# Kernel optimization log

Measured on AMD Instinct MI355X. Metric: run time of the kernel, lower is better.

## Reference

```python
import jax, jax.numpy as jnp
import numpy as np
import math

N = 512            # batch
D = 512            # in_features (embedding dim)
C = 50000          # out_features (num classes)
S = 30.0           # scale
M = 0.5            # margin
COS_M = math.cos(M)
SIN_M = math.sin(M)
TH = math.cos(math.pi - M)
MM = math.sin(math.pi - M) * M


def _l2norm(x, eps=1e-12):
    # torch F.normalize: x / max(||x||_2, eps) along dim=1
    n = jnp.sqrt(jnp.sum(x * x, axis=1, keepdims=True))
    return x / jnp.maximum(n, eps)


def setup_inputs() -> dict:
    key = jax.random.key(0)
    k1, k2, k3 = jax.random.split(key, 3)
    logits = jax.random.normal(k1, (N, D), dtype=jnp.float32)
    labels = jax.random.randint(k2, (N,), 0, C, dtype=jnp.int64)
    # xavier_uniform over (C, D): bound = sqrt(6/(C+D))
    bound = math.sqrt(6.0 / (C + D))
    weight = jax.random.uniform(k3, (C, D), dtype=jnp.float32, minval=-bound, maxval=bound)
    return {"logits": logits, "labels": labels, "weight": weight}


def reference(logits, labels, weight):
    x = _l2norm(logits)                      # [N, D]
    w = _l2norm(weight)                      # [C, D]
    cosine = jnp.einsum('nd,cd->nc', x, w)   # [N, C]
    sine = jnp.sqrt(jnp.clip(1.0 + 1e-7 - cosine * cosine, 0.0, 1.0))
    phi = cosine * COS_M - sine * SIN_M
    # easy_margin=False branch
    phi = jnp.where(cosine > TH, phi, cosine - MM)
    onehot = jax.nn.one_hot(labels, C, dtype=cosine.dtype)  # [N, C]
    output = (onehot * phi + (1.0 - onehot) * cosine) * S
    # CrossEntropyLoss(reduction='none') then .mean()
    logp = jax.nn.log_softmax(output, axis=1)
    loss_per = -jnp.take_along_axis(logp, labels[:, None], axis=1)[:, 0]
    loss = jnp.mean(loss_per)
    return output, loss
```

## Files before the change

### kernel.cpp

```cpp
#include <hip/hip_runtime.h>
#include <stdint.h>

#define N_B   512
#define D_K   512
#define C_N   50000
#define C_PAD 50048
#define BM    256
#define BN    128
#define BK    32
#define NCB   391
#define NWG   (NCB * 2)
#define NT    16

#define S_SCALE 30.0f
#define COS_Mc  0.87758256189037276f
#define SIN_Mc  0.47942553860420301f
#define TH_Cc  (-0.87758256189037276f)
#define MM_Cc   0.23971276930210156f
#define NEG_BIG (-3.0e38f)

typedef __attribute__((ext_vector_type(8))) __bf16 bf16x8;
typedef __attribute__((ext_vector_type(4))) float  f32x4;

__device__ __forceinline__ unsigned short f2bf(float f) {
    union { float f; unsigned u; } v; v.f = f;
    unsigned r = v.u + 0x7FFFu + ((v.u >> 16) & 1u);
    return (unsigned short)(r >> 16);
}

__device__ __forceinline__ void gl2lds16(const void* g, void* l) {
    __builtin_amdgcn_global_load_lds(
        (__attribute__((address_space(1))) unsigned int*)(g),
        (__attribute__((address_space(3))) unsigned int*)(l),
        16, 0, 0);
}

__global__ __launch_bounds__(256) void prep_all_kernel(
        const float* __restrict__ x, unsigned short* __restrict__ xb,
        float* __restrict__ invx,
        const float* __restrict__ w, unsigned short* __restrict__ wb,
        float* __restrict__ invw)
{
    const int wave = threadIdx.x >> 6, lane = threadIdx.x & 63;
    const int l15 = lane & 15, sub = lane >> 4;
    const float* src; unsigned short* dstb; float* inv; int row, nvalid;
    if (blockIdx.x < 32) {
        src = x; dstb = xb; inv = invx; nvalid = N_B;
        row = blockIdx.x * 16 + wave * 4 + sub;
    } else {
        src = w; dstb = wb; inv = invw; nvalid = C_N;
        row = (blockIdx.x - 32) * 16 + wave * 4 + sub;
    }
    unsigned short* drow = dstb + (size_t)row * D_K;
    if (row < nvalid) {
        const float4* s4 = (const float4*)(src + (size_t)row * D_K);
        float4 v[8];
        #pragma unroll
        for (int k = 0; k < 8; k++) v[k] = s4[l15 + 16 * k];
        float ss = 0.f;
        #pragma unroll
        for (int k = 0; k < 8; k++)
            ss += v[k].x * v[k].x + v[k].y * v[k].y
                + v[k].z * v[k].z + v[k].w * v[k].w;
        #pragma unroll
        for (int off = 1; off < 16; off <<= 1) ss += __shfl_xor(ss, off, 64);
        if (l15 == 0) inv[row] = 1.0f / fmaxf(sqrtf(ss), 1e-12f);
        #pragma unroll
        for (int k = 0; k < 8; k++) {
            uint2 o;
            o.x = (unsigned)f2bf(v[k].x) | ((unsigned)f2bf(v[k].y) << 16);
            o.y = (unsigned)f2bf(v[k].z) | ((unsigned)f2bf(v[k].w) << 16);
            *(uint2*)(drow + (l15 + 16 * k) * 4) = o;
        }
    } else {
        uint2 z = make_uint2(0u, 0u);
        #pragma unroll
        for (int k = 0; k < 8; k++) *(uint2*)(drow + (l15 + 16 * k) * 4) = z;
        if (l15 == 0) inv[row] = 0.0f;
    }
}

__global__ __launch_bounds__(512, 4) void gemm_margin_kernel(
        const unsigned short* __restrict__ xb, const unsigned short* __restrict__ wb,
        const float* __restrict__ invx, const float* __restrict__ invw,
        const int* __restrict__ labels, float* __restrict__ out,
        float* __restrict__ m_part, float* __restrict__ s_part)
{
    const int orig = blockIdx.x;
    const int qch = NWG >> 3, rch = NWG & 7;
    const int xcd = orig & 7, idx = orig >> 3;
    const int wg = (xcd < rch ? xcd * (qch + 1)
                              : rch * (qch + 1) + (xcd - rch) * qch) + idx;
    const int cb = wg >> 1, rb = wg & 1;
    const int m0 = rb * BM, c0 = cb * BN;
    const int tid = threadIdx.x;
    const int lane = tid & 63, wave = tid >> 6;
    const int wm = wave >> 1, wn = wave & 1;
    const int l15 = lane & 15, q = lane >> 4;

    __shared__ __align__(16) unsigned short As[2][BM * BK];
    __shared__ __align__(16) unsigned short Bs[2][BN * BK];
    __shared__ float s_invx[BM];
    __shared__ float s_invw[BN];
    __shared__ int   s_lab[BM];
    float* sm  = (float*)&As[0][0];
    float* ssm = sm + 2 * BM;

    f32x4 zero4 = {0.f, 0.f, 0.f, 0.f};
    f32x4 acc[4][4];
    #pragma unroll
    for (int i = 0; i < 4; i++)
        #pragma unroll
        for (int j = 0; j < 4; j++) acc[i][j] = zero4;

    const int srow   = tid >> 2;
    const int pchunk = tid & 3;
    const int lch0 = pchunk ^ ((srow >> 1) & 3);
    const int lch1 = pchunk ^ (((srow + 128) >> 1) & 3);

    const unsigned short* gA0 = xb + (size_t)(m0 + srow)       * D_K + lch0 * 8;
    const unsigned short* gA1 = xb + (size_t)(m0 + srow + 128) * D_K + lch1 * 8;
    const unsigned short* gB0 = wb + (size_t)(c0 + srow)       * D_K + lch0 * 8;

    const int offA0 = srow * BK + pchunk * 8;
    const int offA1 = (srow + 128) * BK + pchunk * 8;
    const int offB0 = srow * BK + pchunk * 8;

    int aoff[4], boff[4];
    #pragma unroll
    for (int i = 0; i < 4; i++) {
        int Ra = wm * 64 + i * 16 + l15;
        aoff[i] = Ra * BK + (q ^ ((Ra >> 1) & 3)) * 8;
        int Rb = wn * 64 + i * 16 + l15;
        boff[i] = Rb * BK + (q ^ ((Rb >> 1) & 3)) * 8;
    }

#define STAGE(b, k0) do {                       \
        gl2lds16(gA0 + (k0), &As[b][offA0]);    \
        gl2lds16(gA1 + (k0), &As[b][offA1]);    \
        gl2lds16(gB0 + (k0), &Bs[b][offB0]);    \
    } while (0)

#define COMPUTE(b) do {                                                       \
        bf16x8 af_[4], bf_[4];                                                \
        _Pragma("unroll")                                                     \
        for (int i = 0; i < 4; i++) af_[i] = *(const bf16x8*)(&As[b][aoff[i]]); \
        _Pragma("unroll")                                                     \
        for (int i = 0; i < 4; i++) bf_[i] = *(const bf16x8*)(&Bs[b][boff[i]]); \
        _Pragma("unroll")                                                     \
        for (int mi = 0; mi < 4; mi++)                                        \
            _Pragma("unroll")                                                 \
            for (int ni = 0; ni < 4; ni++)                                    \
                acc[mi][ni] = __builtin_amdgcn_mfma_f32_16x16x32_bf16(        \
                                  af_[mi], bf_[ni], acc[mi][ni], 0, 0, 0);    \
    } while (0)

    STAGE(0, 0);
    if (tid < BM) {
        s_invx[tid] = invx[m0 + tid];
        s_lab[tid]  = labels[m0 + tid];
    }
    if (tid < BN) s_invw[tid] = invw[c0 + tid];
    __syncthreads();

    #pragma unroll
    for (int t = 0; t < NT; ++t) {
        const int cur = t & 1;
        if (t < NT - 1) STAGE(cur ^ 1, (t + 1) * BK);
        COMPUTE(cur);
        __syncthreads();
    }
#undef STAGE
#undef COMPUTE

    #pragma unroll
    for (int mi = 0; mi < 4; mi++) {
        #pragma unroll
        for (int r = 0; r < 4; r++) {
            int lrow = wm * 64 + mi * 16 + q * 4 + r;
            int grow = m0 + lrow;
            float ivx = s_invx[lrow];
            int lab = s_lab[lrow];
            float tv[4]; bool ok[4];
            float vmax = NEG_BIG;
            #pragma unroll
            for (int ni = 0; ni < 4; ni++) {
                int lcol = wn * 64 + ni * 16 + l15;
                int gcol = c0 + lcol;
                float cosv = acc[mi][ni][r] * ivx * s_invw[lcol];
                float o;
                if (gcol == lab) {
                    float s2 = 1.0f + 1e-7f - cosv * cosv;
                    s2 = fminf(fmaxf(s2, 0.0f), 1.0f);
                    float phi = cosv * COS_Mc - sqrtf(s2) * SIN_Mc;
                    if (!(cosv > TH_Cc)) phi = cosv - MM_Cc;
                    o = S_SCALE * phi;
                } else {
                    o = S_SCALE * cosv;
                }
                ok[ni] = (gcol < C_N);
                tv[ni] = o;
                if (ok[ni]) {
                    out[(size_t)grow * C_N + gcol] = o;
                    vmax = fmaxf(vmax, o);
                }
            }
            #pragma unroll
            for (int off = 1; off < 16; off <<= 1)
                vmax = fmaxf(vmax, __shfl_xor(vmax, off, 64));
            float vs = 0.f;
            #pragma unroll
            for (int ni = 0; ni < 4; ni++)
                if (ok[ni]) vs += __expf(tv[ni] - vmax);
            #pragma unroll
            for (int off = 1; off < 16; off <<= 1)
                vs += __shfl_xor(vs, off, 64);
            if (l15 == 0) { sm[wn * BM + lrow] = vmax; ssm[wn * BM + lrow] = vs; }
        }
    }
    __syncthreads();
    if (tid < BM) {
        float m1 = sm[0 * BM + tid], s1 = ssm[0 * BM + tid];
        float m2 = sm[1 * BM + tid], s2 = ssm[1 * BM + tid];
        float M = fmaxf(m1, m2);
        float S = s1 * __expf(m1 - M) + s2 * __expf(m2 - M);
        m_part[(size_t)(m0 + tid) * NCB + cb] = M;
        s_part[(size_t)(m0 + tid) * NCB + cb] = S;
    }
}

__global__ void rowreduce_kernel(
        const float* __restrict__ m_part, const float* __restrict__ s_part,
        const float* __restrict__ out, const int* __restrict__ labels,
        float* __restrict__ lossp)
{
    int row = blockIdx.x;
    int lane = threadIdx.x;
    float mv[7], sv[7];
    #pragma unroll
    for (int i = 0; i < 7; i++) {
        int j = lane + 64 * i;
        bool in = (j < NCB);
        mv[i] = in ? m_part[(size_t)row * NCB + j] : NEG_BIG;
        sv[i] = in ? s_part[(size_t)row * NCB + j] : 0.f;
    }
    float m = mv[0], s = sv[0];
    #pragma unroll
    for (int i = 1; i < 7; i++) {
        float M = fmaxf(m, mv[i]);
        s = s * __expf(m - M) + sv[i] * __expf(mv[i] - M);
        m = M;
    }
    #pragma unroll
    for (int off = 1; off < 64; off <<= 1) {
        float om = __shfl_xor(m, off, 64);
        float os = __shfl_xor(s, off, 64);
        float M = fmaxf(m, om);
        s = s * __expf(m - M) + os * __expf(om - M);
        m = M;
    }
    if (lane == 0) {
        float logZ = m + logf(s);
        int lab = labels[row];
        lossp[row] = logZ - out[(size_t)row * C_N + lab];
    }
}

__global__ void loss_kernel(const float* __restrict__ lossp, float* __restrict__ loss_out) {
    int t = threadIdx.x;
    float v = lossp[t] + lossp[t + 256];
    #pragma unroll
    for (int off = 32; off >= 1; off >>= 1) v += __shfl_xor(v, off, 64);
    __shared__ float part[4];
    if ((t & 63) == 0) part[t >> 6] = v;
    __syncthreads();
    if (t == 0) loss_out[0] = (part[0] + part[1] + part[2] + part[3]) * (1.0f / 512.0f);
}

extern "C" void kernel_launch(void* const* d_in, const int* in_sizes, int n_in,
                              void* d_out, int out_size, void* d_ws, size_t ws_size,
                              hipStream_t stream)
{
    const float* x      = (const float*)d_in[0];
    const int*   labels = (const int*)d_in[1];
    const float* w      = (const float*)d_in[2];
    float* out = (float*)d_out;
    float* loss_out = out + (size_t)N_B * C_N;

    char* ws = (char*)d_ws;
    size_t off = 0;
    unsigned short* xb = (unsigned short*)(ws + off); off += (size_t)N_B * D_K * 2;
    unsigned short* wb = (unsigned short*)(ws + off); off += (size_t)C_PAD * D_K * 2;
    float* invx   = (float*)(ws + off); off += (size_t)N_B * 4;
    float* invw   = (float*)(ws + off); off += (size_t)C_PAD * 4;
    float* m_part = (float*)(ws + off); off += (size_t)N_B * NCB * 4;
    float* s_part = (float*)(ws + off); off += (size_t)N_B * NCB * 4;
    float* lossp  = (float*)(ws + off); off += (size_t)N_B * 4;

    prep_all_kernel<<<32 + C_PAD / 16, 256, 0, stream>>>(x, xb, invx, w, wb, invw);
    gemm_margin_kernel<<<dim3(NWG), 512, 0, stream>>>(xb, wb, invx, invw, labels,
                                                      out, m_part, s_part);
    rowreduce_kernel<<<N_B, 64, 0, stream>>>(m_part, s_part, out, labels, lossp);
    loss_kernel<<<1, 256, 0, stream>>>(lossp, loss_out);
}
```

Baseline: 244.1 us.

## Fuse weight normalization and bf16 conversion into GEMM B-tile loading

Drops the separate pass that converted the 50000x512 weight matrix to bf16 and computed its inverse norms. The GEMM kernel now loads fp32 weight rows directly into registers, converts them to bf16, writes them to LDS, and accumulates the per-row sum of squares to compute invw after the K loop. This avoids writing and re-reading a ~51MB bf16 copy of the weights. In exchange, B tiles are loaded through registers instead of direct global-to-LDS loads, fp32 weight reads are twice as large, and each weight tile is read by both row-block workgroups.

```diff
diff --git a/kernel.cpp b/kernel.cpp
--- a/kernel.cpp
+++ b/kernel.cpp
@@ -4,7 +4,6 @@
 #define N_B   512
 #define D_K   512
 #define C_N   50000
-#define C_PAD 50048
 #define BM    256
 #define BN    128
 #define BK    32
@@ -35,54 +34,38 @@
         16, 0, 0);
 }
 
-__global__ __launch_bounds__(256) void prep_all_kernel(
+__global__ __launch_bounds__(256) void prep_x_kernel(
         const float* __restrict__ x, unsigned short* __restrict__ xb,
-        float* __restrict__ invx,
-        const float* __restrict__ w, unsigned short* __restrict__ wb,
-        float* __restrict__ invw)
+        float* __restrict__ invx)
 {
     const int wave = threadIdx.x >> 6, lane = threadIdx.x & 63;
     const int l15 = lane & 15, sub = lane >> 4;
-    const float* src; unsigned short* dstb; float* inv; int row, nvalid;
-    if (blockIdx.x < 32) {
-        src = x; dstb = xb; inv = invx; nvalid = N_B;
-        row = blockIdx.x * 16 + wave * 4 + sub;
-    } else {
-        src = w; dstb = wb; inv = invw; nvalid = C_N;
-        row = (blockIdx.x - 32) * 16 + wave * 4 + sub;
-    }
-    unsigned short* drow = dstb + (size_t)row * D_K;
-    if (row < nvalid) {
-        const float4* s4 = (const float4*)(src + (size_t)row * D_K);
-        float4 v[8];
-        #pragma unroll
-        for (int k = 0; k < 8; k++) v[k] = s4[l15 + 16 * k];
-        float ss = 0.f;
-        #pragma unroll
-        for (int k = 0; k < 8; k++)
-            ss += v[k].x * v[k].x + v[k].y * v[k].y
-                + v[k].z * v[k].z + v[k].w * v[k].w;
-        #pragma unroll
-        for (int off = 1; off < 16; off <<= 1) ss += __shfl_xor(ss, off, 64);
-        if (l15 == 0) inv[row] = 1.0f / fmaxf(sqrtf(ss), 1e-12f);
-        #pragma unroll
-        for (int k = 0; k < 8; k++) {
-            uint2 o;
-            o.x = (unsigned)f2bf(v[k].x) | ((unsigned)f2bf(v[k].y) << 16);
-            o.y = (unsigned)f2bf(v[k].z) | ((unsigned)f2bf(v[k].w) << 16);
-            *(uint2*)(drow + (l15 + 16 * k) * 4) = o;
-        }
-    } else {
-        uint2 z = make_uint2(0u, 0u);
-        #pragma unroll
-        for (int k = 0; k < 8; k++) *(uint2*)(drow + (l15 + 16 * k) * 4) = z;
-        if (l15 == 0) inv[row] = 0.0f;
+    const int row = blockIdx.x * 16 + wave * 4 + sub;
+    unsigned short* drow = xb + (size_t)row * D_K;
+    const float4* s4 = (const float4*)(x + (size_t)row * D_K);
+    float4 v[8];
+    #pragma unroll
+    for (int k = 0; k < 8; k++) v[k] = s4[l15 + 16 * k];
+    float ss = 0.f;
+    #pragma unroll
+    for (int k = 0; k < 8; k++)
+        ss += v[k].x * v[k].x + v[k].y * v[k].y
+            + v[k].z * v[k].z + v[k].w * v[k].w;
+    #pragma unroll
+    for (int off = 1; off < 16; off <<= 1) ss += __shfl_xor(ss, off, 64);
+    if (l15 == 0) invx[row] = 1.0f / fmaxf(sqrtf(ss), 1e-12f);
+    #pragma unroll
+    for (int k = 0; k < 8; k++) {
+        uint2 o;
+        o.x = (unsigned)f2bf(v[k].x) | ((unsigned)f2bf(v[k].y) << 16);
+        o.y = (unsigned)f2bf(v[k].z) | ((unsigned)f2bf(v[k].w) << 16);
+        *(uint2*)(drow + (l15 + 16 * k) * 4) = o;
     }
 }
 
 __global__ __launch_bounds__(512, 4) void gemm_margin_kernel(
-        const unsigned short* __restrict__ xb, const unsigned short* __restrict__ wb,
-        const float* __restrict__ invx, const float* __restrict__ invw,
+        const unsigned short* __restrict__ xb, const float* __restrict__ w,
+        const float* __restrict__ invx,
         const int* __restrict__ labels, float* __restrict__ out,
         float* __restrict__ m_part, float* __restrict__ s_part)
 {
@@ -102,6 +85,7 @@
     __shared__ __align__(16) unsigned short Bs[2][BN * BK];
     __shared__ float s_invx[BM];
     __shared__ float s_invw[BN];
+    __shared__ float s_w2[BN];
     __shared__ int   s_lab[BM];
     float* sm  = (float*)&As[0][0];
     float* ssm = sm + 2 * BM;
@@ -120,11 +104,15 @@
 
     const unsigned short* gA0 = xb + (size_t)(m0 + srow)       * D_K + lch0 * 8;
     const unsigned short* gA1 = xb + (size_t)(m0 + srow + 128) * D_K + lch1 * 8;
-    const unsigned short* gB0 = wb + (size_t)(c0 + srow)       * D_K + lch0 * 8;
 
     const int offA0 = srow * BK + pchunk * 8;
     const int offA1 = (srow + 128) * BK + pchunk * 8;
     const int offB0 = srow * BK + pchunk * 8;
+
+    const bool bvalid = (c0 + srow) < C_N;
+    const float* gBf = w + (size_t)(c0 + srow) * D_K + lch0 * 8;
+    float ssB = 0.f;
+    f32x4 nb0 = zero4, nb1 = zero4;
 
     int aoff[4], boff[4];
     #pragma unroll
@@ -135,10 +123,27 @@
         boff[i] = Rb * BK + (q ^ ((Rb >> 1) & 3)) * 8;
     }
 
-#define STAGE(b, k0) do {                       \
-        gl2lds16(gA0 + (k0), &As[b][offA0]);    \
-        gl2lds16(gA1 + (k0), &As[b][offA1]);    \
-        gl2lds16(gB0 + (k0), &Bs[b][offB0]);    \
+#define LOADB(k0) do {                                        \
+        if (bvalid) {                                         \
+            nb0 = *(const f32x4*)(gBf + (k0));                \
+            nb1 = *(const f32x4*)(gBf + (k0) + 4);            \
+        } else { nb0 = zero4; nb1 = zero4; }                  \
+    } while (0)
+
+#define CVTWRITE_B(b) do {                                                    \
+        ssB += nb0[0]*nb0[0] + nb0[1]*nb0[1] + nb0[2]*nb0[2] + nb0[3]*nb0[3]  \
+             + nb1[0]*nb1[0] + nb1[1]*nb1[1] + nb1[2]*nb1[2] + nb1[3]*nb1[3]; \
+        bf16x8 bb;                                                            \
+        bb[0] = (__bf16)nb0[0]; bb[1] = (__bf16)nb0[1];                       \
+        bb[2] = (__bf16)nb0[2]; bb[3] = (__bf16)nb0[3];                       \
+        bb[4] = (__bf16)nb1[0]; bb[5] = (__bf16)nb1[1];                       \
+        bb[6] = (__bf16)nb1[2]; bb[7] = (__bf16)nb1[3];                       \
+        *(bf16x8*)(&Bs[b][offB0]) = bb;                                       \
+    } while (0)
+
+#define STAGE_A(b, k0) do {                         \
+        gl2lds16(gA0 + (k0), &As[b][offA0]);        \
+        gl2lds16(gA1 + (k0), &As[b][offA1]);        \
     } while (0)
 
 #define COMPUTE(b) do {                                                       \
@@ -155,23 +160,37 @@
                                   af_[mi], bf_[ni], acc[mi][ni], 0, 0, 0);    \
     } while (0)
 
-    STAGE(0, 0);
+    LOADB(0);
+    STAGE_A(0, 0);
+    CVTWRITE_B(0);
     if (tid < BM) {
         s_invx[tid] = invx[m0 + tid];
         s_lab[tid]  = labels[m0 + tid];
     }
-    if (tid < BN) s_invw[tid] = invw[c0 + tid];
     __syncthreads();
 
     #pragma unroll
     for (int t = 0; t < NT; ++t) {
         const int cur = t & 1;
-        if (t < NT - 1) STAGE(cur ^ 1, (t + 1) * BK);
+        if (t < NT - 1) { LOADB((t + 1) * BK); STAGE_A(cur ^ 1, (t + 1) * BK); }
         COMPUTE(cur);
+        if (t < NT - 1) CVTWRITE_B(cur ^ 1);
         __syncthreads();
     }
-#undef STAGE
+#undef LOADB
+#undef CVTWRITE_B
+#undef STAGE_A
 #undef COMPUTE
+
+    ssB += __shfl_xor(ssB, 1, 64);
+    ssB += __shfl_xor(ssB, 2, 64);
+    if (pchunk == 0) s_w2[srow] = ssB;
+    __syncthreads();
+    if (tid < BN) {
+        float w2 = s_w2[tid];
+        s_invw[tid] = (w2 > 0.f) ? 1.0f / fmaxf(sqrtf(w2), 1e-12f) : 0.f;
+    }
+    __syncthreads();
 
     #pragma unroll
     for (int mi = 0; mi < 4; mi++) {
@@ -290,15 +309,13 @@
     char* ws = (char*)d_ws;
     size_t off = 0;
     unsigned short* xb = (unsigned short*)(ws + off); off += (size_t)N_B * D_K * 2;
-    unsigned short* wb = (unsigned short*)(ws + off); off += (size_t)C_PAD * D_K * 2;
     float* invx   = (float*)(ws + off); off += (size_t)N_B * 4;
-    float* invw   = (float*)(ws + off); off += (size_t)C_PAD * 4;
     float* m_part = (float*)(ws + off); off += (size_t)N_B * NCB * 4;
     float* s_part = (float*)(ws + off); off += (size_t)N_B * NCB * 4;
     float* lossp  = (float*)(ws + off); off += (size_t)N_B * 4;
 
-    prep_all_kernel<<<32 + C_PAD / 16, 256, 0, stream>>>(x, xb, invx, w, wb, invw);
-    gemm_margin_kernel<<<dim3(NWG), 512, 0, stream>>>(xb, wb, invx, invw, labels,
+    prep_x_kernel<<<32, 256, 0, stream>>>(x, xb, invx);
+    gemm_margin_kernel<<<dim3(NWG), 512, 0, stream>>>(xb, w, invx, labels,
                                                       out, m_part, s_part);
     rowreduce_kernel<<<N_B, 64, 0, stream>>>(m_part, s_part, out, labels, lossp);
     loss_kernel<<<1, 256, 0, stream>>>(lossp, loss_out);
```

After: 378.8 us. 1.55x slower.
